# Optimization experiments

Hardware: AMD Instinct MI355X
Metric: run time of the kernel (lower is better)

The kernel has to match this reference:

```python
import jax, jax.numpy as jnp
import numpy as np

MICRO_BATCHES = 4
NUM_EXPERTS = 8  # world_size=1 -> num_local_experts = 8
EPS = 1e-5


def setup_inputs() -> dict:
    key = jax.random.key(0)
    ks = jax.random.split(key, 8)
    B, S, D = 8, 2048, 1024
    E, F = NUM_EXPERTS, 4 * D
    x = jax.random.normal(ks[0], (B, S, D), dtype=jnp.float32)
    gamma = jnp.ones((D,), jnp.float32)
    beta = jnp.zeros((D,), jnp.float32)
    gate_w = jax.random.normal(ks[1], (E, D), jnp.float32) * (1.0 / np.sqrt(D))
    w1 = jax.random.normal(ks[2], (E, D, F), jnp.float32) * (1.0 / np.sqrt(D))
    b1 = jnp.zeros((E, F), jnp.float32)
    w2 = jax.random.normal(ks[3], (E, F, D), jnp.float32) * (1.0 / np.sqrt(F))
    b2 = jnp.zeros((E, D), jnp.float32)
    return {"x": x, "gamma": gamma, "beta": beta, "gate_w": gate_w,
            "w1": w1, "b1": b1, "w2": w2, "b2": b2}


def reference(x, gamma, beta, gate_w, w1, b1, w2, b2):
    B, S, D = x.shape
    E = w1.shape[0]
    # micro-batch chunking along batch dim (chunk(MICRO_BATCHES, dim=0))
    xf = x.reshape(MICRO_BATCHES, -1, D)            # [MB, T, D], T = B/MB * S
    T = xf.shape[1]
    # residual (gated_input) is the pre-LN flat input
    # moe_norm: LayerNorm over last dim, biased variance, eps=1e-5
    mu = jnp.mean(xf, axis=-1, keepdims=True)
    var = jnp.mean(jnp.square(xf - mu), axis=-1, keepdims=True)
    xn = (xf - mu) * jax.lax.rsqrt(var + EPS) * gamma + beta  # [MB, T, D]
    # gate logits + topk are computed in the source but discarded
    _logits = jnp.einsum('mtd,ed->mte', xn, gate_w)
    _ = jax.lax.top_k(_logits, 2)
    # dispatch/combine are identity for world_size=1; tokens split round-robin
    # into num_local_experts contiguous chunks per micro-batch
    tpe = T // E
    xe = xn.reshape(MICRO_BATCHES, E, tpe, D)       # [MB, E, tpe, D]
    h = jax.nn.gelu(jnp.einsum('metd,edf->metf', xe, w1) + b1[None, :, None, :],
                    approximate=False)
    y = jnp.einsum('metf,efd->metd', h, w2) + b2[None, :, None, :]
    out = xf + y.reshape(MICRO_BATCHES, T, D)       # residual add
    return out.reshape(B, S, D)
```

## Files before the change

### kernel.cpp

```cpp
#include <hip/hip_runtime.h>
#include <stdint.h>
#include <math.h>

typedef unsigned short ushort_t;
typedef __attribute__((ext_vector_type(8))) short bf16x8;
typedef __attribute__((ext_vector_type(4))) float f32x4;

#define SLOT 32768
#define EPI_STRIDE 1032

__device__ __forceinline__ ushort_t f2bf(float f) {
  union { float f; unsigned u; } cv; cv.f = f;
  unsigned r = cv.u + 0x7fffu + ((cv.u >> 16) & 1u);
  return (ushort_t)(r >> 16);
}

__device__ __forceinline__ void gl_lds16(const void* g, void* l) {
  typedef __attribute__((address_space(1))) const char gchar;
  typedef __attribute__((address_space(3))) char lchar;
  __builtin_amdgcn_global_load_lds((gchar*)g, (lchar*)l, 16, 0, 0);
}

__device__ __forceinline__ f32x4 MFMA(bf16x8 a, bf16x8 b, f32x4 c) {
  return __builtin_amdgcn_mfma_f32_16x16x32_bf16(a, b, c, 0, 0, 0);
}

__global__ __launch_bounds__(256) void ln_kernel(const float* __restrict__ x,
                                                 const float* __restrict__ gamma,
                                                 const float* __restrict__ beta,
                                                 ushort_t* __restrict__ xn) {
  const int row = blockIdx.x;
  const int t = threadIdx.x;
  const float4 v = ((const float4*)(x + (size_t)row * 1024))[t];
  float s  = v.x + v.y + v.z + v.w;
  float ss = v.x * v.x + v.y * v.y + v.z * v.z + v.w * v.w;
#pragma unroll
  for (int o = 32; o >= 1; o >>= 1) {
    s  += __shfl_xor(s, o);
    ss += __shfl_xor(ss, o);
  }
  __shared__ float red[10];
  const int wave = t >> 6, lane = t & 63;
  if (lane == 0) { red[wave] = s; red[4 + wave] = ss; }
  __syncthreads();
  if (t == 0) {
    float S  = red[0] + red[1] + red[2] + red[3];
    float SS = red[4] + red[5] + red[6] + red[7];
    float mu  = S * (1.0f / 1024.0f);
    float var = SS * (1.0f / 1024.0f) - mu * mu;
    red[8] = mu;
    red[9] = rsqrtf(var + 1e-5f);
  }
  __syncthreads();
  const float mu = red[8], rs = red[9];
  const float4 g = ((const float4*)gamma)[t];
  const float4 b = ((const float4*)beta)[t];
  ushort4 o;
  o.x = f2bf((v.x - mu) * rs * g.x + b.x);
  o.y = f2bf((v.y - mu) * rs * g.y + b.y);
  o.z = f2bf((v.z - mu) * rs * g.z + b.z);
  o.w = f2bf((v.w - mu) * rs * g.w + b.w);
  ((ushort4*)(xn + (size_t)row * 1024))[t] = o;
}

__global__ __launch_bounds__(256) void transpose_cast(const float* __restrict__ in,
                                                      ushort_t* __restrict__ out,
                                                      int R, int C) {
  __shared__ float tile[32][33];
  const int e = blockIdx.z;
  const float* src = in + (size_t)e * R * C;
  ushort_t* dst = out + (size_t)e * R * C;
  const int c0 = blockIdx.x * 32, r0 = blockIdx.y * 32;
  const int tx = threadIdx.x, ty = threadIdx.y;
#pragma unroll
  for (int j = 0; j < 32; j += 8)
    tile[ty + j][tx] = src[(size_t)(r0 + ty + j) * C + c0 + tx];
  __syncthreads();
#pragma unroll
  for (int j = 0; j < 32; j += 8)
    dst[(size_t)(c0 + ty + j) * R + r0 + tx] = f2bf(tile[tx][ty + j]);
}


__device__ __forceinline__ void stage_half(const ushort_t* gsrc, int lda,
                                           char* half_base, int kt, int tid) {
  const int rr = tid >> 2;
  const int gs = (tid & 3) ^ ((tid >> 3) & 3);
  gl_lds16(gsrc + (size_t)rr * lda + kt + gs * 8, half_base + (tid >> 6) * 1024);
}

template <int BASE>
__device__ __forceinline__ void mfma16(const bf16x8 (&a)[4], const bf16x8 (&b)[4],
                                       f32x4 (&acc)[8][4]) {
  __builtin_amdgcn_s_setprio(1);
#pragma unroll
  for (int mi = 0; mi < 4; mi++)
#pragma unroll
    for (int ni = 0; ni < 4; ni++)
      acc[BASE + mi][ni] = MFMA(a[mi], b[ni], acc[BASE + mi][ni]);
  __builtin_amdgcn_s_setprio(0);
}

template <int SIDX, int VM, bool STG>
__device__ __forceinline__ void slot_body(char* smem, int kt3,
                                          const ushort_t* gA, const ushort_t* gB,
                                          int lda, int a_off, int b_off, int tid,
                                          f32x4 (&acc)[8][4]) {
  const char* slot = smem + SIDX * SLOT;
  char* nstg = smem + ((SIDX + 3) & 3) * SLOT;
  bf16x8 a[4], b[4];
#pragma unroll
  for (int ni = 0; ni < 4; ni++) b[ni] = *(const bf16x8*)(slot + b_off + ni * 1024);
#pragma unroll
  for (int mi = 0; mi < 4; mi++) a[mi] = *(const bf16x8*)(slot + a_off + mi * 1024);
  if (STG) {
    stage_half(gA, lda, nstg, kt3, tid);
    stage_half(gA + (size_t)128 * lda, lda, nstg + 8192, kt3, tid);
  }
  __builtin_amdgcn_sched_barrier(0);
  __builtin_amdgcn_s_barrier();
  asm volatile("s_waitcnt lgkmcnt(0)" ::: "memory");
  __builtin_amdgcn_sched_barrier(0);
  mfma16<0>(a, b, acc);
  __builtin_amdgcn_sched_barrier(0);
  __builtin_amdgcn_s_barrier();
#pragma unroll
  for (int mi = 0; mi < 4; mi++) a[mi] = *(const bf16x8*)(slot + a_off + (mi + 4) * 1024);
  if (STG) {
    stage_half(gB, lda, nstg + 16384, kt3, tid);
    stage_half(gB + (size_t)128 * lda, lda, nstg + 24576, kt3, tid);
  }
  __builtin_amdgcn_sched_barrier(0);
  __builtin_amdgcn_s_barrier();
  asm volatile("s_waitcnt lgkmcnt(0)" ::: "memory");
  __builtin_amdgcn_sched_barrier(0);
  mfma16<4>(a, b, acc);
  __builtin_amdgcn_sched_barrier(0);
  if (VM == 8)      asm volatile("s_waitcnt vmcnt(8)" ::: "memory");
  else if (VM == 4) asm volatile("s_waitcnt vmcnt(4)" ::: "memory");
  else if (VM == 0) asm volatile("s_waitcnt vmcnt(0)" ::: "memory");
  __builtin_amdgcn_s_barrier();
}

template <int EPI, int LDA, int LDC, int KTOT>
__global__ __launch_bounds__(512, 2) void gemm256(const ushort_t* __restrict__ A,
                                                  const ushort_t* __restrict__ Bw,
                                                  const float* __restrict__ bias,
                                                  const float* __restrict__ resid,
                                                  ushort_t* __restrict__ Hout,
                                                  float* __restrict__ Fout) {
  extern __shared__ char smem[];
  const int tid = threadIdx.x;
  const int wave = tid >> 6, lane = tid & 63;

  const int bid = blockIdx.x;
  const int c = bid & 7, l = bid >> 3;
  const int tm = c * 8 + (l & 7);
  const int tn = l >> 3;
  const int row0 = tm * 256;
  const int col0 = tn * 256;
  const int e = (row0 >> 9) & 7;

  const ushort_t* gA = A + (size_t)row0 * LDA;
  const ushort_t* gB = Bw + ((size_t)e * LDC + col0) * LDA;

  const int NT = KTOT / 32;

  const int wm = wave >> 2, wn = wave & 3;
  const int l15 = lane & 15, g = lane >> 4;
  const int sw = ((g ^ ((lane >> 1) & 3)) << 4);
  const int a_off = wm * 8192 + l15 * 64 + sw;
  const int b_off = 16384 + (wn >> 1) * 8192 + (wn & 1) * 4096 + l15 * 64 + sw;

  f32x4 acc[8][4] = {};

#pragma unroll
  for (int T = 0; T < 3; ++T) {
    char* s = smem + T * SLOT;
    stage_half(gA, LDA, s, T * 32, tid);
    stage_half(gA + (size_t)128 * LDA, LDA, s + 8192, T * 32, tid);
    stage_half(gB, LDA, s + 16384, T * 32, tid);
    stage_half(gB + (size_t)128 * LDA, LDA, s + 24576, T * 32, tid);
  }
  asm volatile("s_waitcnt vmcnt(8)" ::: "memory");
  __builtin_amdgcn_s_barrier();

  for (int T = 0; T < NT - 4; T += 4) {
    slot_body<0, 8, true>(smem, (T + 3) * 32, gA, gB, LDA, a_off, b_off, tid, acc);
    slot_body<1, 8, true>(smem, (T + 4) * 32, gA, gB, LDA, a_off, b_off, tid, acc);
    slot_body<2, 8, true>(smem, (T + 5) * 32, gA, gB, LDA, a_off, b_off, tid, acc);
    slot_body<3, 8, true>(smem, (T + 6) * 32, gA, gB, LDA, a_off, b_off, tid, acc);
  }
  slot_body<0, 8, true >(smem, (NT - 1) * 32, gA, gB, LDA, a_off, b_off, tid, acc);
  slot_body<1, 4, false>(smem, 0,             gA, gB, LDA, a_off, b_off, tid, acc);
  slot_body<2, 0, false>(smem, 0,             gA, gB, LDA, a_off, b_off, tid, acc);
  slot_body<3, -1, false>(smem, 0,            gA, gB, LDA, a_off, b_off, tid, acc);

  __syncthreads();

  float bv[4];
#pragma unroll
  for (int ni = 0; ni < 4; ni++)
    bv[ni] = bias[e * LDC + col0 + wn * 64 + ni * 16 + l15];

#pragma unroll
  for (int r = 0; r < 4; ++r) {
#pragma unroll
    for (int mh = 0; mh < 2; ++mh) {
      const int mi = 2 * r + mh;
      const int lrow = wm * 32 + mh * 16 + g * 4;
#pragma unroll
      for (int ni = 0; ni < 4; ++ni) {
        const int colb = (wn * 64 + ni * 16 + l15) * 4;
#pragma unroll
        for (int rr = 0; rr < 4; ++rr) {
          float v = acc[mi][ni][rr] + bv[ni];
          if (EPI == 0) {
            float v2 = v * v;
            float cc = fmaf(0.044715f, v2, 1.0f);
            float u  = exp2f(-2.3022078f * v * cc);
            v = __fdividef(v, 1.0f + u);
          }
          *(float*)(smem + (size_t)(lrow + rr) * EPI_STRIDE + colb) = v;
        }
      }
    }
    __syncthreads();
#pragma unroll
    for (int i = 0; i < 8; ++i) {
      const int chunk = i * 512 + tid;
      const int lr = chunk >> 6;
      const int cb = (chunk & 63) * 16;
      const float4 v4 = *(const float4*)(smem + (size_t)lr * EPI_STRIDE + cb);
      const int grow = row0 + (lr < 32 ? r * 32 + lr : 128 + r * 32 + (lr - 32));
      const int gcol = col0 + (chunk & 63) * 4;
      if (EPI == 0) {
        ushort4 o;
        o.x = f2bf(v4.x); o.y = f2bf(v4.y); o.z = f2bf(v4.z); o.w = f2bf(v4.w);
        *(ushort4*)(&Hout[(size_t)grow * LDC + gcol]) = o;
      } else {
        const float4 rs = *(const float4*)(&resid[(size_t)grow * LDC + gcol]);
        float4 o;
        o.x = v4.x + rs.x; o.y = v4.y + rs.y; o.z = v4.z + rs.z; o.w = v4.w + rs.w;
        *(float4*)(&Fout[(size_t)grow * LDC + gcol]) = o;
      }
    }
    __syncthreads();
  }
}

extern "C" void kernel_launch(void* const* d_in, const int* in_sizes, int n_in,
                              void* d_out, int out_size, void* d_ws, size_t ws_size,
                              hipStream_t stream) {
  const float* x     = (const float*)d_in[0];
  const float* gamma = (const float*)d_in[1];
  const float* beta  = (const float*)d_in[2];
  const float* w1    = (const float*)d_in[4];
  const float* b1    = (const float*)d_in[5];
  const float* w2    = (const float*)d_in[6];
  const float* b2    = (const float*)d_in[7];
  float* out = (float*)d_out;

  char* ws = (char*)d_ws;
  ushort_t* xn  = (ushort_t*)ws;
  ushort_t* w1t = (ushort_t*)(ws + 33554432);
  ushort_t* w2t = (ushort_t*)(ws + 33554432 + 67108864);
  ushort_t* h   = (ushort_t*)(ws + 33554432 + 2 * 67108864);

  hipFuncSetAttribute(reinterpret_cast<const void*>(&gemm256<0, 1024, 4096, 1024>),
                      hipFuncAttributeMaxDynamicSharedMemorySize, 131072);
  hipFuncSetAttribute(reinterpret_cast<const void*>(&gemm256<1, 4096, 1024, 4096>),
                      hipFuncAttributeMaxDynamicSharedMemorySize, 131072);

  ln_kernel<<<16384, 256, 0, stream>>>(x, gamma, beta, xn);
  transpose_cast<<<dim3(128, 32, 8), dim3(32, 8), 0, stream>>>(w1, w1t, 1024, 4096);
  transpose_cast<<<dim3(32, 128, 8), dim3(32, 8), 0, stream>>>(w2, w2t, 4096, 1024);

  gemm256<0, 1024, 4096, 1024><<<dim3(1024), 512, 131072, stream>>>(xn, w1t, b1, nullptr, h, nullptr);
  gemm256<1, 4096, 1024, 4096><<<dim3(256), 512, 131072, stream>>>(h, w2t, b2, x, nullptr, out);
}
```

Before: 425.0 us.

## Prefetch next slot's LDS fragments into registers during current MFMA block

```diff
diff --git a/kernel.cpp b/kernel.cpp
--- a/kernel.cpp
+++ b/kernel.cpp
@@ -101,45 +101,50 @@
   __builtin_amdgcn_s_setprio(0);
 }
 
-template <int SIDX, int VM, bool STG>
+template <int SIDX, int VM, bool STG, bool LAST>
 __device__ __forceinline__ void slot_body(char* smem, int kt3,
                                           const ushort_t* gA, const ushort_t* gB,
                                           int lda, int a_off, int b_off, int tid,
+                                          bf16x8 (&aX)[4], bf16x8 (&aY)[4],
+                                          bf16x8 (&bC)[4], bf16x8 (&bN)[4],
                                           f32x4 (&acc)[8][4]) {
-  const char* slot = smem + SIDX * SLOT;
+  const char* slot  = smem + SIDX * SLOT;
+  const char* nslot = smem + ((SIDX + 1) & 3) * SLOT;
   char* nstg = smem + ((SIDX + 3) & 3) * SLOT;
-  bf16x8 a[4], b[4];
-#pragma unroll
-  for (int ni = 0; ni < 4; ni++) b[ni] = *(const bf16x8*)(slot + b_off + ni * 1024);
-#pragma unroll
-  for (int mi = 0; mi < 4; mi++) a[mi] = *(const bf16x8*)(slot + a_off + mi * 1024);
+#pragma unroll
+  for (int mi = 0; mi < 4; mi++) aY[mi] = *(const bf16x8*)(slot + a_off + (mi + 4) * 1024);
   if (STG) {
     stage_half(gA, lda, nstg, kt3, tid);
     stage_half(gA + (size_t)128 * lda, lda, nstg + 8192, kt3, tid);
   }
   __builtin_amdgcn_sched_barrier(0);
+  asm volatile("s_waitcnt lgkmcnt(4)" ::: "memory");
+  __builtin_amdgcn_sched_barrier(0);
+  mfma16<0>(aX, bC, acc);
+  __builtin_amdgcn_sched_barrier(0);
+  if (VM == 6)      asm volatile("s_waitcnt vmcnt(6)" ::: "memory");
+  else if (VM == 4) asm volatile("s_waitcnt vmcnt(4)" ::: "memory");
+  else if (VM == 0) asm volatile("s_waitcnt vmcnt(0)" ::: "memory");
   __builtin_amdgcn_s_barrier();
-  asm volatile("s_waitcnt lgkmcnt(0)" ::: "memory");
-  __builtin_amdgcn_sched_barrier(0);
-  mfma16<0>(a, b, acc);
-  __builtin_amdgcn_sched_barrier(0);
-  __builtin_amdgcn_s_barrier();
-#pragma unroll
-  for (int mi = 0; mi < 4; mi++) a[mi] = *(const bf16x8*)(slot + a_off + (mi + 4) * 1024);
+  __builtin_amdgcn_sched_barrier(0);
+  if (!LAST) {
+#pragma unroll
+    for (int ni = 0; ni < 4; ni++) bN[ni] = *(const bf16x8*)(nslot + b_off + ni * 1024);
+#pragma unroll
+    for (int mi = 0; mi < 4; mi++) aX[mi] = *(const bf16x8*)(nslot + a_off + mi * 1024);
+  }
   if (STG) {
     stage_half(gB, lda, nstg + 16384, kt3, tid);
     stage_half(gB + (size_t)128 * lda, lda, nstg + 24576, kt3, tid);
   }
   __builtin_amdgcn_sched_barrier(0);
+  if (!LAST) asm volatile("s_waitcnt lgkmcnt(8)" ::: "memory");
+  else       asm volatile("s_waitcnt lgkmcnt(0)" ::: "memory");
+  __builtin_amdgcn_sched_barrier(0);
+  mfma16<4>(aY, bC, acc);
+  __builtin_amdgcn_sched_barrier(0);
   __builtin_amdgcn_s_barrier();
-  asm volatile("s_waitcnt lgkmcnt(0)" ::: "memory");
-  __builtin_amdgcn_sched_barrier(0);
-  mfma16<4>(a, b, acc);
-  __builtin_amdgcn_sched_barrier(0);
-  if (VM == 8)      asm volatile("s_waitcnt vmcnt(8)" ::: "memory");
-  else if (VM == 4) asm volatile("s_waitcnt vmcnt(4)" ::: "memory");
-  else if (VM == 0) asm volatile("s_waitcnt vmcnt(0)" ::: "memory");
-  __builtin_amdgcn_s_barrier();
+  __builtin_amdgcn_sched_barrier(0);
 }
 
 template <int EPI, int LDA, int LDC, int KTOT>
@@ -173,6 +178,7 @@
   const int b_off = 16384 + (wn >> 1) * 8192 + (wn & 1) * 4096 + l15 * 64 + sw;
 
   f32x4 acc[8][4] = {};
+  bf16x8 aX[4], aY[4], bE[4], bO[4];
 
 #pragma unroll
   for (int T = 0; T < 3; ++T) {
@@ -184,17 +190,23 @@
   }
   asm volatile("s_waitcnt vmcnt(8)" ::: "memory");
   __builtin_amdgcn_s_barrier();
+  __builtin_amdgcn_sched_barrier(0);
+#pragma unroll
+  for (int ni = 0; ni < 4; ni++) bE[ni] = *(const bf16x8*)(smem + b_off + ni * 1024);
+#pragma unroll
+  for (int mi = 0; mi < 4; mi++) aX[mi] = *(const bf16x8*)(smem + a_off + mi * 1024);
+  __builtin_amdgcn_sched_barrier(0);
 
   for (int T = 0; T < NT - 4; T += 4) {
-    slot_body<0, 8, true>(smem, (T + 3) * 32, gA, gB, LDA, a_off, b_off, tid, acc);
-    slot_body<1, 8, true>(smem, (T + 4) * 32, gA, gB, LDA, a_off, b_off, tid, acc);
-    slot_body<2, 8, true>(smem, (T + 5) * 32, gA, gB, LDA, a_off, b_off, tid, acc);
-    slot_body<3, 8, true>(smem, (T + 6) * 32, gA, gB, LDA, a_off, b_off, tid, acc);
-  }
-  slot_body<0, 8, true >(smem, (NT - 1) * 32, gA, gB, LDA, a_off, b_off, tid, acc);
-  slot_body<1, 4, false>(smem, 0,             gA, gB, LDA, a_off, b_off, tid, acc);
-  slot_body<2, 0, false>(smem, 0,             gA, gB, LDA, a_off, b_off, tid, acc);
-  slot_body<3, -1, false>(smem, 0,            gA, gB, LDA, a_off, b_off, tid, acc);
+    slot_body<0, 6, true, false>(smem, (T + 3) * 32, gA, gB, LDA, a_off, b_off, tid, aX, aY, bE, bO, acc);
+    slot_body<1, 6, true, false>(smem, (T + 4) * 32, gA, gB, LDA, a_off, b_off, tid, aX, aY, bO, bE, acc);
+    slot_body<2, 6, true, false>(smem, (T + 5) * 32, gA, gB, LDA, a_off, b_off, tid, aX, aY, bE, bO, acc);
+    slot_body<3, 6, true, false>(smem, (T + 6) * 32, gA, gB, LDA, a_off, b_off, tid, aX, aY, bO, bE, acc);
+  }
+  slot_body<0, 6, true,  false>(smem, (NT - 1) * 32, gA, gB, LDA, a_off, b_off, tid, aX, aY, bE, bO, acc);
+  slot_body<1, 4, false, false>(smem, 0,             gA, gB, LDA, a_off, b_off, tid, aX, aY, bO, bE, acc);
+  slot_body<2, 0, false, false>(smem, 0,             gA, gB, LDA, a_off, b_off, tid, aX, aY, bE, bO, acc);
+  slot_body<3, -1, false, true>(smem, 0,             gA, gB, LDA, a_off, b_off, tid, aX, aY, bO, bE, acc);
 
   __syncthreads();
 
```

Result: no change. 427.8 us (+0.7%).
